# Kernel tuning notes

Measured on AMD Instinct MI355X. Metric: run time of the kernel, lower is better.

Reference implementation:

```python
import jax, jax.numpy as jnp
import numpy as np
import math

B, N, E = 256, 512, 2048          # graphs, nodes per graph, edges per graph
EMB = 64                           # emb_sz (must be 64 to match final per-graph matmul with 64-d fc2 output)
NUM_ITEMS, NUM_CATS = 400000, 1000
RATIO = 0.9
EPS = 1e-5


def _bn(x, g, b):
    # BatchNorm1d in training mode: biased batch statistics
    m = x.mean(axis=0)
    v = x.var(axis=0)
    return g * (x - m) * jax.lax.rsqrt(v + EPS) + b


def _graph_conv(x, src, dst, emask, Wr, Wn, b):
    # PyG GraphConv, aggr='add': out_i = lin_root(x_i) + lin_rel(sum_{j->i} x_j) + bias
    msg = jnp.where(emask[:, None], x[src], jnp.zeros((), x.dtype))  # [E_tot, C]
    agg = jnp.zeros_like(x).at[dst].add(msg)
    return agg @ Wn + x @ Wr + b


def _topk_pool(x, src, dst, emask, p, n):
    # TopKPooling: score = x.p/||p||, keep top ceil(ratio*n) per graph, gate with tanh(score)
    k = int(math.ceil(RATIO * n))
    score = x @ p / jnp.linalg.norm(p)                       # [B*n]
    _, idx = jax.lax.top_k(score.reshape(B, n), k)           # [B, k] local indices
    gidx = (idx + (jnp.arange(B) * n)[:, None]).reshape(-1)  # [B*k] global indices
    xk = x[gidx] * jnp.tanh(score[gidx])[:, None]
    # remap edges; edges touching a dropped node become masked-out
    mapping = jnp.full((B * n,), -1, jnp.int32).at[gidx].set(jnp.arange(B * k, dtype=jnp.int32))
    nsrc, ndst = mapping[src], mapping[dst]
    valid = (nsrc >= 0) & (ndst >= 0) & emask
    return xk, jnp.maximum(nsrc, 0), jnp.maximum(ndst, 0), valid, k


def _readout(x, k):
    # uniform graphs: global_max_pool / global_mean_pool via reshape
    xg = x.reshape(B, k, -1)
    return jnp.concatenate([xg.max(axis=1), xg.mean(axis=1)], axis=1)  # [B, 256]


def setup_inputs() -> dict:
    key = jax.random.key(0)
    ks = jax.random.split(key, 32)
    nrm = jax.random.normal
    s = 0.02
    item_id = jax.random.randint(ks[0], (B * N,), 0, NUM_ITEMS)
    cat_id = jax.random.randint(ks[1], (B * N,), 0, NUM_CATS)
    off = (jnp.arange(B, dtype=jnp.int32) * N)[:, None]
    src = (jax.random.randint(ks[2], (B, E), 0, N, dtype=jnp.int32) + off).reshape(-1)
    dst = (jax.random.randint(ks[3], (B, E), 0, N, dtype=jnp.int32) + off).reshape(-1)
    d = dict(
        item_id=item_id, cat_id=cat_id, src=src, dst=dst,
        emb_item=nrm(ks[4], (NUM_ITEMS, EMB)) * s,
        emb_cat=nrm(ks[5], (NUM_CATS, EMB)) * s,
        W1r=nrm(ks[6], (2 * EMB, 128)) * s, W1n=nrm(ks[7], (2 * EMB, 128)) * s, b1=jnp.zeros(128), p1=nrm(ks[8], (128,)),
        W2r=nrm(ks[9], (128, 128)) * s, W2n=nrm(ks[10], (128, 128)) * s, b2=jnp.zeros(128), p2=nrm(ks[11], (128,)),
        W3r=nrm(ks[12], (128, 128)) * s, W3n=nrm(ks[13], (128, 128)) * s, b3=jnp.zeros(128), p3=nrm(ks[14], (128,)),
        fc1_W=nrm(ks[15], (256, 128)) * s, fc1_b=jnp.zeros(128), bn1_g=jnp.ones(128), bn1_b=jnp.zeros(128),
        fc2_W=nrm(ks[16], (128, 64)) * s, fc2_b=jnp.zeros(64), bn2_g=jnp.ones(64), bn2_b=jnp.zeros(64),
    )
    return d


def reference(item_id, cat_id, src, dst, emb_item, emb_cat,
              W1r, W1n, b1, p1, W2r, W2n, b2, p2, W3r, W3n, b3, p3,
              fc1_W, fc1_b, bn1_g, bn1_b, fc2_W, fc2_b, bn2_g, bn2_b):
    e_item = emb_item[item_id]                               # [B*N, 64]
    e_cat = emb_cat[cat_id]                                  # [B*N, 64]
    x = jnp.concatenate([e_item, e_cat], axis=1)             # [B*N, 128]
    emask = jnp.ones(src.shape, bool)

    x = jax.nn.relu(_graph_conv(x, src, dst, emask, W1r, W1n, b1))
    x, src, dst, emask, k1 = _topk_pool(x, src, dst, emask, p1, N)
    x1 = _readout(x, k1)

    x = jax.nn.relu(_graph_conv(x, src, dst, emask, W2r, W2n, b2))
    x, src, dst, emask, k2 = _topk_pool(x, src, dst, emask, p2, k1)
    x2 = _readout(x, k2)

    x = jax.nn.relu(_graph_conv(x, src, dst, emask, W3r, W3n, b3))
    x, src, dst, emask, k3 = _topk_pool(x, src, dst, emask, p3, k2)
    x3 = _readout(x, k3)

    g = x1 + x2 + x3                                         # [B, 256]
    g = jax.nn.relu(_bn(g @ fc1_W + fc1_b, bn1_g, bn1_b))    # fc1
    g = jax.nn.relu(_bn(g @ fc2_W + fc2_b, bn2_g, bn2_b))    # fc2
    # dropout is identity in eval; original applies relu again after dropout
    g = jax.nn.relu(g)                                       # [B, 64]
    # per-graph matmul loop: out[n] = <emb_item[n], g[graph_of_n]>; uniform graphs -> einsum
    out = jnp.einsum('bnd,bd->bn', e_item.reshape(B, N, EMB), g).reshape(-1)
    return jax.nn.sigmoid(out)                               # [B*N]
```

## Files before the change

### kernel.cpp

```cpp
#include <hip/hip_runtime.h>
#include <hip/hip_bf16.h>
#include <math.h>


#define TOTAL_NODES 131072
#define NUM_GRAPHS  256
#define NODES_PER_G 512
#define E_TOTAL     524288
#define EPG         2048
#define FDIM        128
#define EMBD        64

typedef __bf16 bf16x8 __attribute__((ext_vector_type(8)));
typedef float  f32x4  __attribute__((ext_vector_type(4)));

static __device__ __forceinline__ f32x4 mfma16(bf16x8 a, bf16x8 b, f32x4 c) {
  return __builtin_amdgcn_mfma_f32_16x16x32_bf16(a, b, c, 0, 0, 0);
}

static inline size_t align256(size_t x) { return (x + 255) & ~size_t(255); }

__global__ __launch_bounds__(256) void gather_embed_k(
    const int* __restrict__ item_id, const int* __restrict__ cat_id,
    const float* __restrict__ emb_item, const float* __restrict__ emb_cat,
    float* __restrict__ x, int total)
{
  int i = blockIdx.x * 256 + threadIdx.x;
  int node = i >> 5, part = i & 31;
  if (node >= total) return;
  float4 v;
  if (part < 16) {
    v = *(const float4*)&emb_item[(size_t)item_id[node] * EMBD + part * 4];
  } else {
    v = *(const float4*)&emb_cat[(size_t)cat_id[node] * EMBD + (part - 16) * 4];
  }
  *(float4*)&x[(size_t)node * FDIM + part * 4] = v;
}

__global__ __launch_bounds__(256) void wprep_k(
    const float* __restrict__ w0, const float* __restrict__ w1,
    const float* __restrict__ w2, const float* __restrict__ w3,
    const float* __restrict__ w4, const float* __restrict__ w5,
    __bf16* __restrict__ wout)
{
  const float* ws[6] = {w0, w1, w2, w3, w4, w5};
  int mat = blockIdx.y;
  int idx = blockIdx.x * 256 + threadIdx.x;
  int n = idx >> 7, k = idx & 127;
  float v = ws[mat][k * FDIM + n];
  __bf16 h = (__bf16)v;
  __bf16 l = (__bf16)(v - (float)h);
  __bf16* base = wout + (size_t)mat * 2 * 16384;
  base[idx] = h;
  base[16384 + idx] = l;
}

__global__ __launch_bounds__(128) void pnorm3_k(
    const float* __restrict__ p1, const float* __restrict__ p2,
    const float* __restrict__ p3, float* __restrict__ nrm)
{
  __shared__ float ss[128];
  const float* ps[3] = {p1, p2, p3};
  int t = threadIdx.x;
  for (int m = 0; m < 3; ++m) {
    float v = ps[m][t];
    ss[t] = v * v;
    __syncthreads();
    for (int s = 64; s > 0; s >>= 1) {
      if (t < s) ss[t] += ss[t + s];
      __syncthreads();
    }
    if (t == 0) nrm[m] = sqrtf(ss[0]);
    __syncthreads();
  }
}

__global__ __launch_bounds__(512) void csr_build_k(
    const int* __restrict__ src_in, const int* __restrict__ dst_in,
    const int* __restrict__ mapping,
    int* __restrict__ src_out, int* __restrict__ dst_out,
    int* __restrict__ slots, int* __restrict__ counts, int* __restrict__ offs,
    int n_new)
{
  __shared__ int hist[512];
  __shared__ int scan[512];
  __shared__ int cursor[512];
  const int g = blockIdx.x, t = threadIdx.x;
  const int ebase = g * EPG;
  const int nbase = g * n_new;
  hist[t] = 0;
  __syncthreads();
  int ls[4], ld[4];
#pragma unroll
  for (int i = 0; i < 4; ++i) {
    int e = ebase + t + i * 512;
    int s = src_in[e], d = dst_in[e];
    if (mapping) {
      s = (s >= 0) ? mapping[s] : -1;
      d = (d >= 0) ? mapping[d] : -1;
      if (s < 0 || d < 0) { s = -1; d = -1; }
    }
    src_out[e] = s; dst_out[e] = d;
    ls[i] = (s >= 0) ? (s - nbase) : -1;
    ld[i] = (d >= 0) ? (d - nbase) : -1;
    if (ld[i] >= 0) atomicAdd(&hist[ld[i]], 1);
  }
  __syncthreads();
  int v = (t < n_new) ? hist[t] : 0;
  scan[t] = v;
  __syncthreads();
  for (int dlt = 1; dlt < 512; dlt <<= 1) {
    int add = (t >= dlt) ? scan[t - dlt] : 0;
    __syncthreads();
    scan[t] += add;
    __syncthreads();
  }
  if (t < n_new) {
    int excl = scan[t] - v;
    counts[nbase + t] = v;
    offs[nbase + t] = g * EPG + excl;
    cursor[t] = excl;
  }
  __syncthreads();
#pragma unroll
  for (int i = 0; i < 4; ++i) {
    if (ld[i] >= 0) {
      int pos = atomicAdd(&cursor[ld[i]], 1);
      slots[ebase + pos] = ls[i];
    }
  }
}

#define GCH  32
#define GPAD 36
__global__ __launch_bounds__(256) void gather_lds_k(
    const float* __restrict__ x, const int* __restrict__ sel,
    const float* __restrict__ gates, const int* __restrict__ slots,
    const int* __restrict__ off, const int* __restrict__ counts,
    float* __restrict__ agg, int n_per_g)
{
  __shared__ float xs[NODES_PER_G * GPAD];
  const int g = blockIdx.x, ch = blockIdx.y;
  const int tid = threadIdx.x;
  const int c0 = ch * GCH;
  const int rowbase = g * n_per_g;
  const int nv4 = n_per_g * 8;
  for (int v = tid; v < nv4; v += 256) {
    int r = v >> 3, c4 = (v & 7) * 4;
    int srow; float gt;
    if (sel) { srow = sel[rowbase + r]; gt = gates[rowbase + r]; }
    else     { srow = rowbase + r;      gt = 1.0f; }
    float4 t = *(const float4*)&x[(size_t)srow * FDIM + c0 + c4];
    t.x *= gt; t.y *= gt; t.z *= gt; t.w *= gt;
    *(float4*)&xs[r * GPAD + c4] = t;
  }
  __syncthreads();
  const int nlane = tid & 7;
  const int nslot = tid >> 3;
  for (int n = nslot; n < n_per_g; n += 32) {
    int gn = rowbase + n;
    int deg = counts[gn];
    int base = off[gn];
    float4 a = make_float4(0.f, 0.f, 0.f, 0.f);
    for (int d = 0; d < deg; ++d) {
      int s = slots[base + d];
      float4 v = *(const float4*)&xs[s * GPAD + nlane * 4];
      a.x += v.x; a.y += v.y; a.z += v.z; a.w += v.w;
    }
    *(float4*)&agg[(size_t)gn * FDIM + c0 + nlane * 4] = a;
  }
}

__global__ __launch_bounds__(256) void conv_mfma_k(
    const float* __restrict__ Asrc, const int* __restrict__ sel,
    const float* __restrict__ gates,
    const __bf16* __restrict__ W1hl,
    const float* __restrict__ A2,
    const __bf16* __restrict__ W2hl,
    const float* __restrict__ bias, const float* __restrict__ p,
    const float* __restrict__ nrm, float* __restrict__ C,
    float* __restrict__ score, int M)
{
  __shared__ __bf16 Wh[128 * 72];
  __shared__ __bf16 Wl[128 * 72];

  const int tid  = threadIdx.x;
  const int lane = tid & 63;
  const int w    = tid >> 6;
  const int row0 = blockIdx.x * 128;
  const int l15  = lane & 15;
  const int lg   = lane >> 4;

  f32x4 acc[2][8];
#pragma unroll
  for (int rf = 0; rf < 2; ++rf)
#pragma unroll
    for (int cf = 0; cf < 8; ++cf) acc[rf][cf] = (f32x4){0.f, 0.f, 0.f, 0.f};

  const int grow0 = row0 + w * 32 + l15;
  const int grow1 = grow0 + 16;

  for (int pass = 0; pass < 2; ++pass) {
    const float* __restrict__ A = pass ? A2 : Asrc;
    const __bf16* __restrict__ Whl = pass ? W2hl : W1hl;
    const bool use_sel = (pass == 0) && (sel != nullptr);
    int srow0 = use_sel ? sel[grow0] : grow0;
    int srow1 = use_sel ? sel[grow1] : grow1;
    float gt0 = use_sel ? gates[grow0] : 1.0f;
    float gt1 = use_sel ? gates[grow1] : 1.0f;

    for (int half = 0; half < 2; ++half) {
      const int k0 = half * 64;
      __syncthreads();
      for (int v = tid; v < 1024; v += 256) {
        int c = v >> 3, chn = (v & 7) * 8;
        *(bf16x8*)&Wh[c * 72 + chn] = *(const bf16x8*)&Whl[c * 128 + k0 + chn];
        *(bf16x8*)&Wl[c * 72 + chn] = *(const bf16x8*)&Whl[16384 + c * 128 + k0 + chn];
      }
      __syncthreads();

      bf16x8 ah[2][2], al[2][2];
#pragma unroll
      for (int rf = 0; rf < 2; ++rf) {
        int srow = rf ? srow1 : srow0;
        float gt = rf ? gt1 : gt0;
#pragma unroll
        for (int kc = 0; kc < 2; ++kc) {
          const float* ap = &A[(size_t)srow * FDIM + k0 + kc * 32 + lg * 8];
          float4 u0 = *(const float4*)ap;
          float4 u1 = *(const float4*)(ap + 4);
          float av[8] = {u0.x, u0.y, u0.z, u0.w, u1.x, u1.y, u1.z, u1.w};
#pragma unroll
          for (int j = 0; j < 8; ++j) {
            float vv = av[j] * gt;
            __bf16 h = (__bf16)vv;
            ah[rf][kc][j] = h;
            al[rf][kc][j] = (__bf16)(vv - (float)h);
          }
        }
      }
#pragma unroll
      for (int kc = 0; kc < 2; ++kc) {
        const int koff = kc * 32 + lg * 8;
#pragma unroll
        for (int cf = 0; cf < 8; ++cf) {
          const int bo = (cf * 16 + l15) * 72 + koff;
          bf16x8 bh = *(const bf16x8*)&Wh[bo];
          bf16x8 bl = *(const bf16x8*)&Wl[bo];
          acc[0][cf] = mfma16(ah[0][kc], bh, acc[0][cf]);
          acc[0][cf] = mfma16(ah[0][kc], bl, acc[0][cf]);
          acc[0][cf] = mfma16(al[0][kc], bh, acc[0][cf]);
          acc[1][cf] = mfma16(ah[1][kc], bh, acc[1][cf]);
          acc[1][cf] = mfma16(ah[1][kc], bl, acc[1][cf]);
          acc[1][cf] = mfma16(al[1][kc], bh, acc[1][cf]);
        }
      }
    }
  }

  const float nv = nrm[0];
  float bv[8], pv[8];
#pragma unroll
  for (int cf = 0; cf < 8; ++cf) {
    int col = cf * 16 + l15;
    bv[cf] = bias[col];
    pv[cf] = p[col];
  }
#pragma unroll
  for (int rf = 0; rf < 2; ++rf) {
#pragma unroll
    for (int j = 0; j < 4; ++j) {
      int row = row0 + w * 32 + rf * 16 + lg * 4 + j;
      float* crow = &C[(size_t)row * FDIM];
      float rsv = 0.f;
#pragma unroll
      for (int cf = 0; cf < 8; ++cf) {
        float val = acc[rf][cf][j] + bv[cf];
        val = fmaxf(val, 0.f);
        crow[cf * 16 + l15] = val;
        rsv += val * pv[cf];
      }
      rsv += __shfl_xor(rsv, 1, 16);
      rsv += __shfl_xor(rsv, 2, 16);
      rsv += __shfl_xor(rsv, 4, 16);
      rsv += __shfl_xor(rsv, 8, 16);
      if (l15 == 0) score[row] = rsv / nv;
    }
  }
}

__global__ __launch_bounds__(512) void topk_sort_k(
    const float* __restrict__ score, int n_old, int k_new,
    int* __restrict__ sel, int* __restrict__ mapping, float* __restrict__ gates)
{
  __shared__ float sv[512];
  __shared__ int   si[512];
  int b = blockIdx.x, t = threadIdx.x;
  sv[t] = (t < n_old) ? -score[(size_t)b * n_old + t] : 3.0e38f;
  si[t] = t;
  __syncthreads();
  for (int k = 2; k <= 512; k <<= 1) {
    for (int j = k >> 1; j > 0; j >>= 1) {
      int ixj = t ^ j;
      if (ixj > t) {
        bool up = ((t & k) == 0);
        float a = sv[t], c = sv[ixj];
        if ((a > c) == up) {
          sv[t] = c; sv[ixj] = a;
          int tmp = si[t]; si[t] = si[ixj]; si[ixj] = tmp;
        }
      }
      __syncthreads();
    }
  }
  if (t < n_old) {
    int old_g = b * n_old + si[t];
    if (t < k_new) {
      sel[b * k_new + t] = old_g;
      mapping[old_g] = b * k_new + t;
      gates[b * k_new + t] = tanhf(-sv[t]);
    } else {
      mapping[old_g] = -1;
    }
  }
}

__global__ __launch_bounds__(256) void readout_k(
    const float* __restrict__ x, const int* __restrict__ sel,
    const float* __restrict__ gates, float* __restrict__ g, int k)
{
  __shared__ float lmx[32 * 36];
  __shared__ float lsm[32 * 36];
  const int b = blockIdx.x, ch = blockIdx.y;
  const int c0 = ch * 32;
  const int tid = threadIdx.x;
  const int lane = tid & 7;
  const int slot = tid >> 3;
  float4 mx = make_float4(-3.0e38f, -3.0e38f, -3.0e38f, -3.0e38f);
  float4 sm = make_float4(0.f, 0.f, 0.f, 0.f);
  for (int n = slot; n < k; n += 32) {
    int node = b * k + n;
    int old = sel[node];
    float gate = gates[node];
    float4 v = *(const float4*)&x[(size_t)old * FDIM + c0 + lane * 4];
    v.x *= gate; v.y *= gate; v.z *= gate; v.w *= gate;
    mx.x = fmaxf(mx.x, v.x); mx.y = fmaxf(mx.y, v.y);
    mx.z = fmaxf(mx.z, v.z); mx.w = fmaxf(mx.w, v.w);
    sm.x += v.x; sm.y += v.y; sm.z += v.z; sm.w += v.w;
  }
  float* pm = &lmx[slot * 36 + lane * 4];
  float* ps = &lsm[slot * 36 + lane * 4];
  pm[0] = mx.x; pm[1] = mx.y; pm[2] = mx.z; pm[3] = mx.w;
  ps[0] = sm.x; ps[1] = sm.y; ps[2] = sm.z; ps[3] = sm.w;
  __syncthreads();
  for (int s = 16; s > 0; s >>= 1) {
    if (slot < s) {
#pragma unroll
      for (int j = 0; j < 4; ++j) {
        int a = slot * 36 + lane * 4 + j;
        int bb = (slot + s) * 36 + lane * 4 + j;
        lmx[a] = fmaxf(lmx[a], lmx[bb]);
        lsm[a] += lsm[bb];
      }
    }
    __syncthreads();
  }
  if (slot == 0) {
    float inv_k = 1.f / (float)k;
#pragma unroll
    for (int j = 0; j < 4; ++j) {
      int c = c0 + lane * 4 + j;
      g[b * 256 + c]       += lmx[lane * 4 + j];
      g[b * 256 + 128 + c] += lsm[lane * 4 + j] * inv_k;
    }
  }
}

__global__ __launch_bounds__(256) void head1_k(
    const float* __restrict__ g, const float* __restrict__ W,
    const float* __restrict__ bias, const float* __restrict__ gamma,
    const float* __restrict__ beta, float* __restrict__ h1)
{
  __shared__ float wsl[256 * 8];
  __shared__ float rsum[256 * 9];
  __shared__ float rsq[256 * 9];
  const int c0 = blockIdx.x * 8;
  const int t = threadIdx.x;
#pragma unroll
  for (int j = 0; j < 8; ++j) wsl[t * 8 + j] = W[t * 128 + c0 + j];
  __syncthreads();
  float acc[8] = {0.f, 0.f, 0.f, 0.f, 0.f, 0.f, 0.f, 0.f};
  const float* grow = &g[t * 256];
#pragma unroll
  for (int k = 0; k < 256; k += 4) {
    float4 gv = *(const float4*)&grow[k];
#pragma unroll
    for (int j = 0; j < 8; ++j) {
      acc[j] += gv.x * wsl[(k + 0) * 8 + j] + gv.y * wsl[(k + 1) * 8 + j]
              + gv.z * wsl[(k + 2) * 8 + j] + gv.w * wsl[(k + 3) * 8 + j];
    }
  }
#pragma unroll
  for (int j = 0; j < 8; ++j) {
    acc[j] += bias[c0 + j];
    rsum[t * 9 + j] = acc[j];
    rsq[t * 9 + j] = acc[j] * acc[j];
  }
  __syncthreads();
  for (int s = 128; s > 0; s >>= 1) {
    if (t < s) {
#pragma unroll
      for (int j = 0; j < 8; ++j) {
        rsum[t * 9 + j] += rsum[(t + s) * 9 + j];
        rsq[t * 9 + j]  += rsq[(t + s) * 9 + j];
      }
    }
    __syncthreads();
  }
#pragma unroll
  for (int j = 0; j < 8; ++j) {
    float m = rsum[j] * (1.f / 256.f);
    float var = rsq[j] * (1.f / 256.f) - m * m;
    float o = gamma[c0 + j] * (acc[j] - m) * rsqrtf(var + 1e-5f) + beta[c0 + j];
    h1[t * 128 + c0 + j] = fmaxf(o, 0.f);
  }
}

__global__ __launch_bounds__(256) void head2_k(
    const float* __restrict__ h1, const float* __restrict__ W,
    const float* __restrict__ bias, const float* __restrict__ gamma,
    const float* __restrict__ beta, float* __restrict__ h2)
{
  __shared__ float wsl[128 * 8];
  __shared__ float rsum[256 * 9];
  __shared__ float rsq[256 * 9];
  const int c0 = blockIdx.x * 8;
  const int t = threadIdx.x;
  if (t < 128) {
#pragma unroll
    for (int j = 0; j < 8; ++j) wsl[t * 8 + j] = W[t * 64 + c0 + j];
  }
  __syncthreads();
  float acc[8] = {0.f, 0.f, 0.f, 0.f, 0.f, 0.f, 0.f, 0.f};
  const float* hrow = &h1[t * 128];
#pragma unroll
  for (int k = 0; k < 128; k += 4) {
    float4 gv = *(const float4*)&hrow[k];
#pragma unroll
    for (int j = 0; j < 8; ++j) {
      acc[j] += gv.x * wsl[(k + 0) * 8 + j] + gv.y * wsl[(k + 1) * 8 + j]
              + gv.z * wsl[(k + 2) * 8 + j] + gv.w * wsl[(k + 3) * 8 + j];
    }
  }
#pragma unroll
  for (int j = 0; j < 8; ++j) {
    acc[j] += bias[c0 + j];
    rsum[t * 9 + j] = acc[j];
    rsq[t * 9 + j] = acc[j] * acc[j];
  }
  __syncthreads();
  for (int s = 128; s > 0; s >>= 1) {
    if (t < s) {
#pragma unroll
      for (int j = 0; j < 8; ++j) {
        rsum[t * 9 + j] += rsum[(t + s) * 9 + j];
        rsq[t * 9 + j]  += rsq[(t + s) * 9 + j];
      }
    }
    __syncthreads();
  }
#pragma unroll
  for (int j = 0; j < 8; ++j) {
    float m = rsum[j] * (1.f / 256.f);
    float var = rsq[j] * (1.f / 256.f) - m * m;
    float o = gamma[c0 + j] * (acc[j] - m) * rsqrtf(var + 1e-5f) + beta[c0 + j];
    h2[t * 64 + c0 + j] = fmaxf(o, 0.f);
  }
}

__global__ __launch_bounds__(256) void final_k(
    const int* __restrict__ item_id, const float* __restrict__ emb_item,
    const float* __restrict__ g2, float* __restrict__ out, int total)
{
  int nid = blockIdx.x * 256 + threadIdx.x;
  if (nid >= total) return;
  int b = nid >> 9;
  const float* e = &emb_item[(size_t)item_id[nid] * EMBD];
  const float* gg = &g2[(size_t)b * 64];
  float s = 0.f;
#pragma unroll
  for (int j = 0; j < 64; j += 4) {
    float4 a = *(const float4*)&e[j];
    float4 c = *(const float4*)&gg[j];
    s += a.x * c.x + a.y * c.y + a.z * c.z + a.w * c.w;
  }
  out[nid] = 1.f / (1.f + expf(-s));
}

extern "C" void kernel_launch(void* const* d_in, const int* in_sizes, int n_in,
                              void* d_out, int out_size, void* d_ws, size_t ws_size,
                              hipStream_t stream)
{
  const int*   item_id  = (const int*)  d_in[0];
  const int*   cat_id   = (const int*)  d_in[1];
  const int*   src_in   = (const int*)  d_in[2];
  const int*   dst_in   = (const int*)  d_in[3];
  const float* emb_item = (const float*)d_in[4];
  const float* emb_cat  = (const float*)d_in[5];
  const float* W1r = (const float*)d_in[6];
  const float* W1n = (const float*)d_in[7];
  const float* b1  = (const float*)d_in[8];
  const float* p1  = (const float*)d_in[9];
  const float* W2r = (const float*)d_in[10];
  const float* W2n = (const float*)d_in[11];
  const float* b2  = (const float*)d_in[12];
  const float* p2  = (const float*)d_in[13];
  const float* W3r = (const float*)d_in[14];
  const float* W3n = (const float*)d_in[15];
  const float* b3  = (const float*)d_in[16];
  const float* p3  = (const float*)d_in[17];
  const float* fc1_W = (const float*)d_in[18];
  const float* fc1_b = (const float*)d_in[19];
  const float* bn1_g = (const float*)d_in[20];
  const float* bn1_b = (const float*)d_in[21];
  const float* fc2_W = (const float*)d_in[22];
  const float* fc2_b = (const float*)d_in[23];
  const float* bn2_g = (const float*)d_in[24];
  const float* bn2_b = (const float*)d_in[25];
  float* out = (float*)d_out;

  const int TN = TOTAL_NODES;
  const int E  = E_TOTAL;
  const int k1 = 461, k2 = 415, k3 = 374;
  const int M1 = TN;
  const int M2 = NUM_GRAPHS * k1;
  const int M3 = NUM_GRAPHS * k2;

  char* ws = (char*)d_ws;
  size_t off = 0;
  auto carve = [&](size_t bytes) { char* p = ws + off; off += align256(bytes); return p; };
  float*  buf0   = (float*) carve((size_t)TN * FDIM * 4);
  float*  buf1   = (float*) carve((size_t)TN * FDIM * 4);
  float*  score  = (float*) carve((size_t)TN * 4);
  int*    sel    = (int*)   carve((size_t)TN * 4);
  int*    mapping= (int*)   carve((size_t)TN * 4);
  float*  gates  = (float*) carve((size_t)TN * 4);
  int*    srcw   = (int*)   carve((size_t)E * 4);
  int*    dstw   = (int*)   carve((size_t)E * 4);
  int*    counts = (int*)   carve((size_t)TN * 4);
  int*    offs   = (int*)   carve((size_t)TN * 4);
  int*    slots  = (int*)   carve((size_t)E * 4);
  __bf16* wbuf   = (__bf16*)carve(6 * 2 * 16384 * 2);
  float*  g      = (float*) carve(256 * 256 * 4);
  float*  h1     = (float*) carve(256 * 128 * 4);
  float*  h2     = (float*) carve(256 * 64 * 4);
  float*  nrm    = (float*) carve(256);
  if (off > ws_size) return;

  dim3 b256(256);
  auto blocks = [](long long work, int bs) { return dim3((unsigned)((work + bs - 1) / bs)); };

  const __bf16* W1r_hl = wbuf + 0 * 2 * 16384;
  const __bf16* W1n_hl = wbuf + 1 * 2 * 16384;
  const __bf16* W2r_hl = wbuf + 2 * 2 * 16384;
  const __bf16* W2n_hl = wbuf + 3 * 2 * 16384;
  const __bf16* W3r_hl = wbuf + 4 * 2 * 16384;
  const __bf16* W3n_hl = wbuf + 5 * 2 * 16384;

  hipMemsetAsync(g, 0, 256 * 256 * 4, stream);
  wprep_k<<<dim3(64, 6), b256, 0, stream>>>(W1r, W1n, W2r, W2n, W3r, W3n, wbuf);
  pnorm3_k<<<dim3(1), dim3(128), 0, stream>>>(p1, p2, p3, nrm);
  gather_embed_k<<<blocks((long long)TN * 32, 256), b256, 0, stream>>>(
      item_id, cat_id, emb_item, emb_cat, buf0, TN);

  csr_build_k<<<dim3(NUM_GRAPHS), dim3(512), 0, stream>>>(
      src_in, dst_in, nullptr, srcw, dstw, slots, counts, offs, NODES_PER_G);
  gather_lds_k<<<dim3(NUM_GRAPHS, 4), b256, 0, stream>>>(
      buf0, nullptr, nullptr, slots, offs, counts, buf1, NODES_PER_G);
  conv_mfma_k<<<dim3(M1 / 128), b256, 0, stream>>>(
      buf0, nullptr, nullptr, W1r_hl, buf1, W1n_hl, b1, p1, nrm + 0, buf0, score, M1);
  topk_sort_k<<<dim3(NUM_GRAPHS), dim3(512), 0, stream>>>(
      score, NODES_PER_G, k1, sel, mapping, gates);
  readout_k<<<dim3(NUM_GRAPHS, 4), b256, 0, stream>>>(buf0, sel, gates, g, k1);

  csr_build_k<<<dim3(NUM_GRAPHS), dim3(512), 0, stream>>>(
      srcw, dstw, mapping, srcw, dstw, slots, counts, offs, k1);
  gather_lds_k<<<dim3(NUM_GRAPHS, 4), b256, 0, stream>>>(
      buf0, sel, gates, slots, offs, counts, buf1, k1);
  conv_mfma_k<<<dim3(M2 / 128), b256, 0, stream>>>(
      buf0, sel, gates, W2r_hl, buf1, W2n_hl, b2, p2, nrm + 1, buf1, score, M2);
  topk_sort_k<<<dim3(NUM_GRAPHS), dim3(512), 0, stream>>>(
      score, k1, k2, sel, mapping, gates);
  readout_k<<<dim3(NUM_GRAPHS, 4), b256, 0, stream>>>(buf1, sel, gates, g, k2);

  csr_build_k<<<dim3(NUM_GRAPHS), dim3(512), 0, stream>>>(
      srcw, dstw, mapping, srcw, dstw, slots, counts, offs, k2);
  gather_lds_k<<<dim3(NUM_GRAPHS, 4), b256, 0, stream>>>(
      buf1, sel, gates, slots, offs, counts, buf0, k2);
  conv_mfma_k<<<dim3(M3 / 128), b256, 0, stream>>>(
      buf1, sel, gates, W3r_hl, buf0, W3n_hl, b3, p3, nrm + 2, buf0, score, M3);
  topk_sort_k<<<dim3(NUM_GRAPHS), dim3(512), 0, stream>>>(
      score, k2, k3, sel, mapping, gates);
  readout_k<<<dim3(NUM_GRAPHS, 4), b256, 0, stream>>>(buf0, sel, gates, g, k3);

  head1_k<<<dim3(16), b256, 0, stream>>>(g, fc1_W, fc1_b, bn1_g, bn1_b, h1);
  head2_k<<<dim3(8), b256, 0, stream>>>(h1, fc2_W, fc2_b, bn2_g, bn2_b, h2);

  final_k<<<blocks(TN, 256), b256, 0, stream>>>(item_id, emb_item, h2, out, TN);
}
```

Measured before the change: 473.5 us.

## Replace LDS-staged neighbor aggregation with direct global gather using packed source/gate slots

The CSR build now stores, for each edge, the original source row index (resolved through the top-k selection) and its tanh gate as one int2. The LDS-tiled gather kernel, which staged a whole graph's 32-column slice before summing, is replaced by a one-thread-per-float4 kernel that reads neighbor rows straight from global memory and applies the gate per edge. This removes the LDS staging pass and its syncthreads, and lifts the parallelism limit of 1024 blocks. In exchange, neighbor reads become scattered global/L2 accesses and the slot array is twice as large.

```diff
diff --git a/kernel.cpp b/kernel.cpp
--- a/kernel.cpp
+++ b/kernel.cpp
@@ -78,9 +78,11 @@
 __global__ __launch_bounds__(512) void csr_build_k(
     const int* __restrict__ src_in, const int* __restrict__ dst_in,
     const int* __restrict__ mapping,
+    const int* __restrict__ sel_,
+    const float* __restrict__ gates_,
     int* __restrict__ src_out, int* __restrict__ dst_out,
-    int* __restrict__ slots, int* __restrict__ counts, int* __restrict__ offs,
-    int n_new)
+    int2* __restrict__ slot_pack, int* __restrict__ counts,
+    int* __restrict__ offs, int n_new)
 {
   __shared__ int hist[512];
   __shared__ int scan[512];
@@ -126,49 +128,32 @@
   for (int i = 0; i < 4; ++i) {
     if (ld[i] >= 0) {
       int pos = atomicAdd(&cursor[ld[i]], 1);
-      slots[ebase + pos] = ls[i];
-    }
-  }
-}
-
-#define GCH  32
-#define GPAD 36
-__global__ __launch_bounds__(256) void gather_lds_k(
-    const float* __restrict__ x, const int* __restrict__ sel,
-    const float* __restrict__ gates, const int* __restrict__ slots,
+      int sg = nbase + ls[i];
+      int oldr = sel_ ? sel_[sg] : sg;
+      float gt = gates_ ? gates_[sg] : 1.0f;
+      slot_pack[ebase + pos] = make_int2(oldr, __float_as_int(gt));
+    }
+  }
+}
+
+__global__ __launch_bounds__(256) void gather_direct_k(
+    const float* __restrict__ x, const int2* __restrict__ slot_pack,
     const int* __restrict__ off, const int* __restrict__ counts,
-    float* __restrict__ agg, int n_per_g)
-{
-  __shared__ float xs[NODES_PER_G * GPAD];
-  const int g = blockIdx.x, ch = blockIdx.y;
-  const int tid = threadIdx.x;
-  const int c0 = ch * GCH;
-  const int rowbase = g * n_per_g;
-  const int nv4 = n_per_g * 8;
-  for (int v = tid; v < nv4; v += 256) {
-    int r = v >> 3, c4 = (v & 7) * 4;
-    int srow; float gt;
-    if (sel) { srow = sel[rowbase + r]; gt = gates[rowbase + r]; }
-    else     { srow = rowbase + r;      gt = 1.0f; }
-    float4 t = *(const float4*)&x[(size_t)srow * FDIM + c0 + c4];
-    t.x *= gt; t.y *= gt; t.z *= gt; t.w *= gt;
-    *(float4*)&xs[r * GPAD + c4] = t;
-  }
-  __syncthreads();
-  const int nlane = tid & 7;
-  const int nslot = tid >> 3;
-  for (int n = nslot; n < n_per_g; n += 32) {
-    int gn = rowbase + n;
-    int deg = counts[gn];
-    int base = off[gn];
-    float4 a = make_float4(0.f, 0.f, 0.f, 0.f);
-    for (int d = 0; d < deg; ++d) {
-      int s = slots[base + d];
-      float4 v = *(const float4*)&xs[s * GPAD + nlane * 4];
-      a.x += v.x; a.y += v.y; a.z += v.z; a.w += v.w;
-    }
-    *(float4*)&agg[(size_t)gn * FDIM + c0 + nlane * 4] = a;
-  }
+    float* __restrict__ agg, int M)
+{
+  int i = blockIdx.x * 256 + threadIdx.x;
+  int node = i >> 5, lane = i & 31;
+  if (node >= M) return;
+  int deg = counts[node];
+  int base = off[node];
+  float4 a = make_float4(0.f, 0.f, 0.f, 0.f);
+  for (int d = 0; d < deg; ++d) {
+    int2 sp = slot_pack[base + d];
+    float gt = __int_as_float(sp.y);
+    float4 v = *(const float4*)&x[(size_t)sp.x * FDIM + lane * 4];
+    a.x += gt * v.x; a.y += gt * v.y; a.z += gt * v.z; a.w += gt * v.w;
+  }
+  *(float4*)&agg[(size_t)node * FDIM + lane * 4] = a;
 }
 
 __global__ __launch_bounds__(256) void conv_mfma_k(
@@ -549,7 +534,7 @@
   int*    dstw   = (int*)   carve((size_t)E * 4);
   int*    counts = (int*)   carve((size_t)TN * 4);
   int*    offs   = (int*)   carve((size_t)TN * 4);
-  int*    slots  = (int*)   carve((size_t)E * 4);
+  int2*   slotp  = (int2*)  carve((size_t)E * 8);
   __bf16* wbuf   = (__bf16*)carve(6 * 2 * 16384 * 2);
   float*  g      = (float*) carve(256 * 256 * 4);
   float*  h1     = (float*) carve(256 * 128 * 4);
@@ -574,9 +559,10 @@
       item_id, cat_id, emb_item, emb_cat, buf0, TN);
 
   csr_build_k<<<dim3(NUM_GRAPHS), dim3(512), 0, stream>>>(
-      src_in, dst_in, nullptr, srcw, dstw, slots, counts, offs, NODES_PER_G);
-  gather_lds_k<<<dim3(NUM_GRAPHS, 4), b256, 0, stream>>>(
-      buf0, nullptr, nullptr, slots, offs, counts, buf1, NODES_PER_G);
+      src_in, dst_in, nullptr, nullptr, nullptr,
+      srcw, dstw, slotp, counts, offs, NODES_PER_G);
+  gather_direct_k<<<blocks((long long)M1 * 32, 256), b256, 0, stream>>>(
+      buf0, slotp, offs, counts, buf1, M1);
   conv_mfma_k<<<dim3(M1 / 128), b256, 0, stream>>>(
       buf0, nullptr, nullptr, W1r_hl, buf1, W1n_hl, b1, p1, nrm + 0, buf0, score, M1);
   topk_sort_k<<<dim3(NUM_GRAPHS), dim3(512), 0, stream>>>(
@@ -584,9 +570,10 @@
   readout_k<<<dim3(NUM_GRAPHS, 4), b256, 0, stream>>>(buf0, sel, gates, g, k1);
 
   csr_build_k<<<dim3(NUM_GRAPHS), dim3(512), 0, stream>>>(
-      srcw, dstw, mapping, srcw, dstw, slots, counts, offs, k1);
-  gather_lds_k<<<dim3(NUM_GRAPHS, 4), b256, 0, stream>>>(
-      buf0, sel, gates, slots, offs, counts, buf1, k1);
+      srcw, dstw, mapping, sel, gates,
+      srcw, dstw, slotp, counts, offs, k1);
+  gather_direct_k<<<blocks((long long)M2 * 32, 256), b256, 0, stream>>>(
+      buf0, slotp, offs, counts, buf1, M2);
   conv_mfma_k<<<dim3(M2 / 128), b256, 0, stream>>>(
       buf0, sel, gates, W2r_hl, buf1, W2n_hl, b2, p2, nrm + 1, buf1, score, M2);
   topk_sort_k<<<dim3(NUM_GRAPHS), dim3(512), 0, stream>>>(
@@ -594,9 +581,10 @@
   readout_k<<<dim3(NUM_GRAPHS, 4), b256, 0, stream>>>(buf1, sel, gates, g, k2);
 
   csr_build_k<<<dim3(NUM_GRAPHS), dim3(512), 0, stream>>>(
-      srcw, dstw, mapping, srcw, dstw, slots, counts, offs, k2);
-  gather_lds_k<<<dim3(NUM_GRAPHS, 4), b256, 0, stream>>>(
-      buf1, sel, gates, slots, offs, counts, buf0, k2);
+      srcw, dstw, mapping, sel, gates,
+      srcw, dstw, slotp, counts, offs, k2);
+  gather_direct_k<<<blocks((long long)M3 * 32, 256), b256, 0, stream>>>(
+      buf1, slotp, offs, counts, buf0, M3);
   conv_mfma_k<<<dim3(M3 / 128), b256, 0, stream>>>(
       buf1, sel, gates, W3r_hl, buf0, W3n_hl, b3, p3, nrm + 2, buf0, score, M3);
   topk_sort_k<<<dim3(NUM_GRAPHS), dim3(512), 0, stream>>>(
```

Result: faster. 409.0 us (-13.6%).
